# Performance work log

Measured on AMD Instinct MI355X. Metric: run time of the kernel, lower is better.

## Reference

```python
import jax, jax.numpy as jnp
import numpy as np

HID, KQ, V = 1024, 64, 64
B, S = 8, 2048
NEG_INF = -1000000000.0


def setup_inputs() -> dict:
    key = jax.random.key(0)
    ks = jax.random.split(key, 10)
    return {
        "k_hidden_inputs": jax.random.normal(ks[0], (B, S, HID), jnp.float32),
        "q_hidden_inputs": jax.random.normal(ks[1], (B, S, HID), jnp.float32),
        "v_hidden_inputs": jax.random.normal(ks[2], (B, S, HID), jnp.float32),
        "mask": jax.random.randint(ks[3], (B, S, S), 0, 2, jnp.int32),
        "Wq": jax.random.normal(ks[4], (HID, KQ), jnp.float32) * 0.02,
        "bq": jnp.zeros((KQ,), jnp.float32),
        "Wk": jax.random.normal(ks[5], (HID, KQ), jnp.float32) * 0.02,
        "bk": jnp.zeros((KQ,), jnp.float32),
        "Wv": jax.random.normal(ks[6], (HID, V), jnp.float32) * 0.02,
        "bv": jnp.zeros((V,), jnp.float32),
    }


def reference(k_hidden_inputs, q_hidden_inputs, v_hidden_inputs, mask,
              Wq, bq, Wk, bk, Wv, bv):
    keys = jnp.einsum('bsh,hd->bsd', k_hidden_inputs, Wk) + bk
    queries = jnp.einsum('bsh,hd->bsd', q_hidden_inputs, Wq) + bq
    values = jnp.einsum('bsh,hd->bsd', v_hidden_inputs, Wv) + bv
    # scaled dot-product scores: [B, S_q, S_k]
    scores = jnp.einsum('bqd,bkd->bqk', queries, keys) / jnp.sqrt(jnp.float32(KQ))
    scores = jnp.where(mask == 0, jnp.float32(NEG_INF), scores)
    attn = jax.nn.softmax(scores, axis=-1)
    return jnp.einsum('bqk,bkv->bqv', attn, values)
```

## Files before the change

### kernel.cpp

```cpp
#include <hip/hip_runtime.h>

#define HIDDEN 1024
#define NB 8
#define SEQ 2048
#define DH 64

typedef long long i64;
typedef unsigned short u16;
typedef __attribute__((ext_vector_type(8))) _Float16 half8;
typedef __attribute__((ext_vector_type(4))) float f32x4;

#define MFMA16F __builtin_amdgcn_mfma_f32_16x16x32_f16

__device__ __forceinline__ u16 f2h(float x) {
    _Float16 h = (_Float16)x;
    return __builtin_bit_cast(u16, h);
}
__device__ __forceinline__ void gl_lds16(const void* g, void* l) {
    __builtin_amdgcn_global_load_lds(
        (const __attribute__((address_space(1))) unsigned int*)g,
        (__attribute__((address_space(3))) unsigned int*)l, 16, 0, 0);
}

__global__ __launch_bounds__(256) void wimg_prep16(
    const float* __restrict__ Wq, const float* __restrict__ Wk, const float* __restrict__ Wv,
    u16* __restrict__ Wimg)
{
    const int t = blockIdx.x * 256 + threadIdx.x;
    const int te = t >> 13;
    const int rem = t & 8191;
    const int p = rem >> 9;
    const int rem2 = rem & 511;
    const int n = rem2 >> 3;
    const int pos = rem2 & 7;
    const float* W = te == 0 ? Wq : te == 1 ? Wk : Wv;
    const int g = pos ^ (n & 7);
    const int k0 = p * 64 + g * 8;
    u16* dst = Wimg + (i64)t * 8;
    #pragma unroll
    for (int j = 0; j < 8; ++j)
        dst[j] = f2h(W[(i64)(k0 + j) * DH + n]);
}

__global__ __launch_bounds__(64) void proj_mfma11(
    const float* __restrict__ qh, const float* __restrict__ kh, const float* __restrict__ vh,
    const u16* __restrict__ Wimg,
    const float* __restrict__ bq, const float* __restrict__ bk, const float* __restrict__ bv,
    u16* __restrict__ Qb, u16* __restrict__ Kb, u16* __restrict__ Vt)
{
    const int te = blockIdx.y;
    const float* A    = te == 0 ? qh : te == 1 ? kh : vh;
    const float* bias = te == 0 ? bq : te == 1 ? bk : bv;
    const int row0 = blockIdx.x << 4;
    const int lane = threadIdx.x;
    const int lr = lane & 15, lg = lane >> 4;

    __shared__ __attribute__((aligned(16))) float AL[5][1024];
    __shared__ __attribute__((aligned(16))) u16  WL[2][4096];

    const u16* Wte = Wimg + (i64)te * 16 * 4096;

    const float* asrc[4];
    #pragma unroll
    for (int i = 0; i < 4; ++i) {
        const int ar = 4 * i + (lane >> 4);
        const int ab = (lane & 15) ^ (ar & 15);
        asrc[i] = A + (i64)(row0 + ar) * HIDDEN + (ab << 2);
    }
    const u16* wsrc = Wte + (lane << 3);

    f32x4 acc[4] = {};

#define STAGE_A(S, B) { \
        _Pragma("unroll") \
        for (int i_ = 0; i_ < 4; ++i_) \
            gl_lds16(asrc[i_] + (S) * 64, &AL[B][i_ * 256]); }
#define STAGE_W(S, B) { \
        _Pragma("unroll") \
        for (int j_ = 0; j_ < 8; ++j_) \
            gl_lds16(wsrc + (S) * 4096 + j_ * 512, &WL[B][j_ * 512]); }

#define COMPUTE(AB, WB) { \
        _Pragma("unroll") \
        for (int ks = 0; ks < 2; ++ks) { \
            const int b0 = ks * 8 + lg * 2; \
            const float4 fa = *(const float4*)&AL[AB][lr * 64 + ((b0 ^ lr) << 2)]; \
            const float4 fb = *(const float4*)&AL[AB][lr * 64 + (((b0 + 1) ^ lr) << 2)]; \
            half8 a; \
            a[0] = (_Float16)fa.x; a[1] = (_Float16)fa.y; \
            a[2] = (_Float16)fa.z; a[3] = (_Float16)fa.w; \
            a[4] = (_Float16)fb.x; a[5] = (_Float16)fb.y; \
            a[6] = (_Float16)fb.z; a[7] = (_Float16)fb.w; \
            _Pragma("unroll") \
            for (int nt = 0; nt < 4; ++nt) { \
                const int n = nt * 16 + lr; \
                const int pos = (ks * 4 + lg) ^ (n & 7); \
                const half8 b = *(const half8*)&WL[WB][n * 64 + (pos << 3)]; \
                acc[nt] = MFMA16F(a, b, acc[nt], 0, 0, 0); \
            } \
        } }

    STAGE_A(0, 0) STAGE_A(1, 1) STAGE_A(2, 2) STAGE_A(3, 3)
    STAGE_W(0, 0)

    STAGE_W(1, 1)
    STAGE_A(4, 4)
    asm volatile("s_waitcnt vmcnt(12)" ::: "memory");
    COMPUTE(0, 0)

    int ab_use = 1, ab_stage = 0;
    #pragma unroll 1
    for (int s = 1; s < 12; ++s) {
        STAGE_W(s + 1, (s + 1) & 1)
        STAGE_A(s + 4, ab_stage)
        asm volatile("s_waitcnt vmcnt(16)" ::: "memory");
        COMPUTE(ab_use, s & 1)
        if (++ab_use == 5) ab_use = 0;
        if (++ab_stage == 5) ab_stage = 0;
    }

    STAGE_W(13, 1)
    asm volatile("s_waitcnt vmcnt(12)" ::: "memory");
    COMPUTE(2, 0)
    STAGE_W(14, 0)
    asm volatile("s_waitcnt vmcnt(8)" ::: "memory");
    COMPUTE(3, 1)
    STAGE_W(15, 1)
    asm volatile("s_waitcnt vmcnt(8)" ::: "memory");
    COMPUTE(4, 0)
    asm volatile("s_waitcnt vmcnt(0)" ::: "memory");
    COMPUTE(0, 1)

#undef STAGE_A
#undef STAGE_W
#undef COMPUTE

    #pragma unroll
    for (int nt = 0; nt < 4; ++nt) {
        const int col = nt * 16 + lr;
        const float bb = bias[col];
        #pragma unroll
        for (int r = 0; r < 4; ++r) {
            const i64 grow = row0 + (lg << 2) + r;
            const u16 v = f2h(acc[nt][r] + bb);
            if (te == 0)      Qb[grow * DH + col] = v;
            else if (te == 1) Kb[grow * DH + col] = v;
            else {
                const i64 bb2 = grow >> 11, key = grow & 2047;
                Vt[(bb2 * DH + col) * SEQ + key] = v;
            }
        }
    }
}

__global__ __launch_bounds__(64) void attn_mfma(
    const u16* __restrict__ Qb, const u16* __restrict__ Kb, const u16* __restrict__ Vt,
    const int* __restrict__ mask, float* __restrict__ out)
{
    __shared__ __attribute__((aligned(16))) u16 Kl[2][64 * 64];
    __shared__ __attribute__((aligned(16))) u16 Vl[2][64 * 64];
    __shared__ __attribute__((aligned(16))) u16 Pl[16][72];

    const int lane = threadIdx.x;
    const int lr = lane & 15, lg = lane >> 4;
    const int b  = blockIdx.x >> 7;
    const int q0 = (blockIdx.x & 127) << 4;

    const i64 qrow = (i64)b * SEQ + q0 + lr;
    const half8 qf0 = *(const half8*)(Qb + qrow * DH + lg * 8);
    const half8 qf1 = *(const half8*)(Qb + qrow * DH + 32 + lg * 8);

    const int srow = lane >> 3;
    const int scb  = lane & 7;

    f32x4 oacc[4] = {};
    float rs0 = 0.f, rs1 = 0.f, rs2 = 0.f, rs3 = 0.f;

    {
        const i64 kbase = (i64)b * SEQ;
        #pragma unroll
        for (int i = 0; i < 8; ++i) {
            int row = i * 8 + srow, cb = scb ^ (row & 7);
            gl_lds16(Kb + (kbase + row) * DH + cb * 8, &Kl[0][i * 512]);
        }
        #pragma unroll
        for (int i = 0; i < 8; ++i) {
            int row = i * 8 + srow, cb = scb ^ (row & 7);
            gl_lds16(Vt + ((i64)b * DH + row) * SEQ + cb * 8, &Vl[0][i * 512]);
        }
    }

    #pragma unroll 1
    for (int t = 0; t < 32; ++t) {
        const int kt = t * 64;
        const int buf = t & 1;

        int mv[16];
        #pragma unroll
        for (int tt = 0; tt < 4; ++tt)
            #pragma unroll
            for (int r = 0; r < 4; ++r)
                mv[tt * 4 + r] =
                    mask[((i64)b * SEQ + q0 + lg * 4 + r) * SEQ + kt + tt * 16 + lr];

        if (t < 31) {
            const int kn = kt + 64;
            const i64 kbase = (i64)b * SEQ + kn;
            #pragma unroll
            for (int i = 0; i < 8; ++i) {
                int row = i * 8 + srow, cb = scb ^ (row & 7);
                gl_lds16(Kb + (kbase + row) * DH + cb * 8, &Kl[buf ^ 1][i * 512]);
            }
            #pragma unroll
            for (int i = 0; i < 8; ++i) {
                int row = i * 8 + srow, cb = scb ^ (row & 7);
                gl_lds16(Vt + ((i64)b * DH + row) * SEQ + kn + cb * 8, &Vl[buf ^ 1][i * 512]);
            }
            asm volatile("s_waitcnt vmcnt(32)" ::: "memory");
        } else {
            asm volatile("s_waitcnt vmcnt(16)" ::: "memory");
        }

        f32x4 sacc[4] = {};
        #pragma unroll
        for (int tt = 0; tt < 4; ++tt) {
            int row = tt * 16 + lr, x = row & 7;
            half8 k0 = *(const half8*)&Kl[buf][row * 64 + ((lg) ^ x) * 8];
            half8 k1 = *(const half8*)&Kl[buf][row * 64 + ((lg + 4) ^ x) * 8];
            sacc[tt] = MFMA16F(qf0, k0, sacc[tt], 0, 0, 0);
            sacc[tt] = MFMA16F(qf1, k1, sacc[tt], 0, 0, 0);
        }

        #pragma unroll
        for (int tt = 0; tt < 4; ++tt) {
            #pragma unroll
            for (int r = 0; r < 4; ++r) {
                float p = (mv[tt * 4 + r] != 0) ? __expf(sacc[tt][r] * 0.125f) : 0.0f;
                if      (r == 0) rs0 += p;
                else if (r == 1) rs1 += p;
                else if (r == 2) rs2 += p;
                else             rs3 += p;
                Pl[lg * 4 + r][tt * 16 + lr] = f2h(p);
            }
        }

        const half8 p0 = *(const half8*)&Pl[lr][lg * 8];
        const half8 p1 = *(const half8*)&Pl[lr][32 + lg * 8];
        #pragma unroll
        for (int vt = 0; vt < 4; ++vt) {
            int row = vt * 16 + lr, x = row & 7;
            half8 v0 = *(const half8*)&Vl[buf][row * 64 + ((lg) ^ x) * 8];
            half8 v1 = *(const half8*)&Vl[buf][row * 64 + ((lg + 4) ^ x) * 8];
            oacc[vt] = MFMA16F(p0, v0, oacc[vt], 0, 0, 0);
            oacc[vt] = MFMA16F(p1, v1, oacc[vt], 0, 0, 0);
        }
    }

    float rs[4] = {rs0, rs1, rs2, rs3};
    #pragma unroll
    for (int r = 0; r < 4; ++r) {
        float v = rs[r];
        v += __shfl_xor(v, 1, 64);
        v += __shfl_xor(v, 2, 64);
        v += __shfl_xor(v, 4, 64);
        v += __shfl_xor(v, 8, 64);
        rs[r] = 1.0f / v;
    }
    #pragma unroll
    for (int vt = 0; vt < 4; ++vt)
        #pragma unroll
        for (int r = 0; r < 4; ++r)
            out[((i64)b * SEQ + q0 + lg * 4 + r) * DH + vt * 16 + lr] = oacc[vt][r] * rs[r];
}

extern "C" void kernel_launch(void* const* d_in, const int* in_sizes, int n_in,
                              void* d_out, int out_size, void* d_ws, size_t ws_size,
                              hipStream_t stream) {
    const float* kh   = (const float*)d_in[0];
    const float* qh   = (const float*)d_in[1];
    const float* vh   = (const float*)d_in[2];
    const int*   mask = (const int*)  d_in[3];
    const float* Wq   = (const float*)d_in[4];
    const float* bq   = (const float*)d_in[5];
    const float* Wk   = (const float*)d_in[6];
    const float* bk   = (const float*)d_in[7];
    const float* Wv   = (const float*)d_in[8];
    const float* bv   = (const float*)d_in[9];
    float* out = (float*)d_out;

    u16* Wimg = (u16*)d_ws;
    u16* Qb   = Wimg + 3 * 16 * 4096;
    u16* Kb   = Qb + (i64)NB * SEQ * DH;
    u16* Vt   = Kb + (i64)NB * SEQ * DH;

    wimg_prep16<<<96, 256, 0, stream>>>(Wq, Wk, Wv, Wimg);
    proj_mfma11<<<dim3(1024, 3), 64, 0, stream>>>(qh, kh, vh, Wimg,
                                                  bq, bk, bv, Qb, Kb, Vt);
    attn_mfma<<<1024, 64, 0, stream>>>(Qb, Kb, Vt, mask, out);
}
```

Before: 126.5 us.

## Restructure projection GEMM into 4-wave 32-row blocks with shared weight tiles

The projection kernel moves from one wave per 16-row block to four waves covering a 32-row by 64-column tile. Each wave handles a 16x32 sub-tile. The weight tile in LDS is now shared across twice as many rows, which halves the weight traffic per output row. The deep 5-stage A ring and its hand-tuned waitcnt schedule are replaced by a simple double buffer with __syncthreads each step. That simpler pipeline waits for vmcnt(0) every iteration, so load latency is less well hidden.

```diff
diff --git a/kernel.cpp b/kernel.cpp
--- a/kernel.cpp
+++ b/kernel.cpp
@@ -42,7 +42,7 @@
         dst[j] = f2h(W[(i64)(k0 + j) * DH + n]);
 }
 
-__global__ __launch_bounds__(64) void proj_mfma11(
+__global__ __launch_bounds__(256) void proj_mfma12(
     const float* __restrict__ qh, const float* __restrict__ kh, const float* __restrict__ vh,
     const u16* __restrict__ Wimg,
     const float* __restrict__ bq, const float* __restrict__ bk, const float* __restrict__ bv,
@@ -51,97 +51,85 @@
     const int te = blockIdx.y;
     const float* A    = te == 0 ? qh : te == 1 ? kh : vh;
     const float* bias = te == 0 ? bq : te == 1 ? bk : bv;
-    const int row0 = blockIdx.x << 4;
-    const int lane = threadIdx.x;
+    const int row0 = blockIdx.x << 5;
+    const int t = threadIdx.x;
+    const int w = t >> 6, lane = t & 63;
     const int lr = lane & 15, lg = lane >> 4;
-
-    __shared__ __attribute__((aligned(16))) float AL[5][1024];
-    __shared__ __attribute__((aligned(16))) u16  WL[2][4096];
+    const int wr = (w & 1) << 4;
+    const int wc = (w >> 1) << 5;
+
+    __shared__ __attribute__((aligned(16))) float AL[2][32 * 64];
+    __shared__ __attribute__((aligned(16))) u16  WL[2][64 * 64];
 
     const u16* Wte = Wimg + (i64)te * 16 * 4096;
 
-    const float* asrc[4];
-    #pragma unroll
-    for (int i = 0; i < 4; ++i) {
-        const int ar = 4 * i + (lane >> 4);
+    const float* asrc[2]; int adst[2];
+    #pragma unroll
+    for (int i = 0; i < 2; ++i) {
+        const int ar = 8 * w + 4 * i + (lane >> 4);
         const int ab = (lane & 15) ^ (ar & 15);
         asrc[i] = A + (i64)(row0 + ar) * HIDDEN + (ab << 2);
-    }
-    const u16* wsrc = Wte + (lane << 3);
-
-    f32x4 acc[4] = {};
-
-#define STAGE_A(S, B) { \
+        adst[i] = (8 * w + 4 * i) * 64;
+    }
+    const u16* wsrc[2]; int wdst[2];
+    #pragma unroll
+    for (int j = 0; j < 2; ++j) {
+        const int n0 = 16 * w + 8 * j;
+        wsrc[j] = Wte + n0 * 64 + (lane << 3);
+        wdst[j] = n0 * 64;
+    }
+
+    f32x4 acc[2] = {};
+
+#define STAGE(P, B) { \
         _Pragma("unroll") \
-        for (int i_ = 0; i_ < 4; ++i_) \
-            gl_lds16(asrc[i_] + (S) * 64, &AL[B][i_ * 256]); }
-#define STAGE_W(S, B) { \
+        for (int i_ = 0; i_ < 2; ++i_) \
+            gl_lds16(asrc[i_] + (P) * 64, &AL[B][adst[i_]]); \
         _Pragma("unroll") \
-        for (int j_ = 0; j_ < 8; ++j_) \
-            gl_lds16(wsrc + (S) * 4096 + j_ * 512, &WL[B][j_ * 512]); }
-
-#define COMPUTE(AB, WB) { \
+        for (int j_ = 0; j_ < 2; ++j_) \
+            gl_lds16(wsrc[j_] + (P) * 4096, &WL[B][wdst[j_]]); }
+
+#define COMPUTE(B) { \
         _Pragma("unroll") \
         for (int ks = 0; ks < 2; ++ks) { \
             const int b0 = ks * 8 + lg * 2; \
-            const float4 fa = *(const float4*)&AL[AB][lr * 64 + ((b0 ^ lr) << 2)]; \
-            const float4 fb = *(const float4*)&AL[AB][lr * 64 + (((b0 + 1) ^ lr) << 2)]; \
+            const float4 fa = *(const float4*)&AL[B][(wr + lr) * 64 + ((b0 ^ lr) << 2)]; \
+            const float4 fb = *(const float4*)&AL[B][(wr + lr) * 64 + (((b0 + 1) ^ lr) << 2)]; \
             half8 a; \
             a[0] = (_Float16)fa.x; a[1] = (_Float16)fa.y; \
             a[2] = (_Float16)fa.z; a[3] = (_Float16)fa.w; \
             a[4] = (_Float16)fb.x; a[5] = (_Float16)fb.y; \
             a[6] = (_Float16)fb.z; a[7] = (_Float16)fb.w; \
             _Pragma("unroll") \
-            for (int nt = 0; nt < 4; ++nt) { \
-                const int n = nt * 16 + lr; \
+            for (int nt = 0; nt < 2; ++nt) { \
+                const int n = wc + nt * 16 + lr; \
                 const int pos = (ks * 4 + lg) ^ (n & 7); \
-                const half8 b = *(const half8*)&WL[WB][n * 64 + (pos << 3)]; \
+                const half8 b = *(const half8*)&WL[B][n * 64 + (pos << 3)]; \
                 acc[nt] = MFMA16F(a, b, acc[nt], 0, 0, 0); \
             } \
         } }
 
-    STAGE_A(0, 0) STAGE_A(1, 1) STAGE_A(2, 2) STAGE_A(3, 3)
-    STAGE_W(0, 0)
-
-    STAGE_W(1, 1)
-    STAGE_A(4, 4)
-    asm volatile("s_waitcnt vmcnt(12)" ::: "memory");
-    COMPUTE(0, 0)
-
-    int ab_use = 1, ab_stage = 0;
+    STAGE(0, 0)
+
+    int buf = 0;
     #pragma unroll 1
-    for (int s = 1; s < 12; ++s) {
-        STAGE_W(s + 1, (s + 1) & 1)
-        STAGE_A(s + 4, ab_stage)
-        asm volatile("s_waitcnt vmcnt(16)" ::: "memory");
-        COMPUTE(ab_use, s & 1)
-        if (++ab_use == 5) ab_use = 0;
-        if (++ab_stage == 5) ab_stage = 0;
-    }
-
-    STAGE_W(13, 1)
-    asm volatile("s_waitcnt vmcnt(12)" ::: "memory");
-    COMPUTE(2, 0)
-    STAGE_W(14, 0)
-    asm volatile("s_waitcnt vmcnt(8)" ::: "memory");
-    COMPUTE(3, 1)
-    STAGE_W(15, 1)
-    asm volatile("s_waitcnt vmcnt(8)" ::: "memory");
-    COMPUTE(4, 0)
-    asm volatile("s_waitcnt vmcnt(0)" ::: "memory");
-    COMPUTE(0, 1)
-
-#undef STAGE_A
-#undef STAGE_W
+    for (int p = 0; p < 16; ++p) {
+        asm volatile("s_waitcnt vmcnt(0)" ::: "memory");
+        __syncthreads();
+        if (p < 15) STAGE(p + 1, buf ^ 1)
+        COMPUTE(buf)
+        buf ^= 1;
+    }
+#undef STAGE
 #undef COMPUTE
 
     #pragma unroll
-    for (int nt = 0; nt < 4; ++nt) {
-        const int col = nt * 16 + lr;
+    for (int nt = 0; nt < 2; ++nt) {
+        const int col = wc + nt * 16 + lr;
         const float bb = bias[col];
         #pragma unroll
         for (int r = 0; r < 4; ++r) {
-            const i64 grow = row0 + (lg << 2) + r;
+            const i64 grow = row0 + wr + (lg << 2) + r;
             const u16 v = f2h(acc[nt][r] + bb);
             if (te == 0)      Qb[grow * DH + col] = v;
             else if (te == 1) Kb[grow * DH + col] = v;
@@ -294,7 +282,7 @@
     u16* Vt   = Kb + (i64)NB * SEQ * DH;
 
     wimg_prep16<<<96, 256, 0, stream>>>(Wq, Wk, Wv, Wimg);
-    proj_mfma11<<<dim3(1024, 3), 64, 0, stream>>>(qh, kh, vh, Wimg,
+    proj_mfma12<<<dim3(512, 3), 256, 0, stream>>>(qh, kh, vh, Wimg,
                                                   bq, bk, bv, Qb, Kb, Vt);
     attn_mfma<<<1024, 64, 0, stream>>>(Qb, Kb, Vt, mask, out);
 }
```

Result: faster. 116.5 us (-7.9%).
